# Kernel tuning notes

Hardware: AMD Instinct MI355X
Metric: run time of the kernel (lower is better)

The kernel has to match this reference:

```python
import jax, jax.numpy as jnp
import numpy as np

B, T, F, K = 32, 1500, 512, 31
QBITS = 8
EPS = 1e-5


def fake_quant(x, bits=QBITS):
    """Symmetric per-tensor fake quantization (scale from dynamic max-abs),
    with straight-through estimator so gradients pass through unchanged."""
    qmax = 2.0 ** (bits - 1) - 1.0  # 127 for 8 bits
    scale = jnp.maximum(jnp.max(jnp.abs(x)) / qmax, 1e-8)
    q = jnp.clip(jnp.round(x / scale), -qmax - 1.0, qmax) * scale
    return x + jax.lax.stop_gradient(q - x)


def setup_inputs() -> dict:
    key = jax.random.key(0)
    ks = jax.random.split(key, 5)
    x = jax.random.normal(ks[0], (B, T, F), dtype=jnp.float32)
    W1 = jax.random.normal(ks[1], (2 * F, F), dtype=jnp.float32) * (1.0 / np.sqrt(F))
    b1 = jnp.zeros((2 * F,), jnp.float32)
    dw_w = jax.random.normal(ks[2], (F, 1, K), dtype=jnp.float32) * (1.0 / np.sqrt(K))
    dw_b = jnp.zeros((F,), jnp.float32)
    W2 = jax.random.normal(ks[3], (F, F), dtype=jnp.float32) * (1.0 / np.sqrt(F))
    b2 = jnp.zeros((F,), jnp.float32)
    return {
        "x": x,
        "ln_gamma": jnp.ones((F,), jnp.float32),
        "ln_beta": jnp.zeros((F,), jnp.float32),
        "W1": W1, "b1": b1,
        "dw_w": dw_w, "dw_b": dw_b,
        "bn_gamma": jnp.ones((F,), jnp.float32),
        "bn_beta": jnp.zeros((F,), jnp.float32),
        "W2": W2, "b2": b2,
    }


def _forward(x, ln_gamma, ln_beta, W1, b1, dw_w, dw_b, bn_gamma, bn_beta, W2, b2):
    # LayerNorm over last dim F
    mu = jnp.mean(x, axis=-1, keepdims=True)
    var = jnp.mean(jnp.square(x - mu), axis=-1, keepdims=True)
    t = (x - mu) * jax.lax.rsqrt(var + EPS) * ln_gamma + ln_beta

    # pconv1 in-quant -> quantized pointwise conv1 (Linear F -> 2F) -> out-quant
    t = fake_quant(t)
    t = jnp.einsum("btf,gf->btg", t, fake_quant(W1)) + b1
    t = fake_quant(t)

    # GLU over last dim: [B,T,2F] -> [B,T,F]
    a, g = jnp.split(t, 2, axis=-1)
    t = a * jax.nn.sigmoid(g)

    # depthwise conv on [B,F,T]
    t = jnp.transpose(t, (0, 2, 1))  # [B,F,T]
    t = fake_quant(t)
    t = jax.lax.conv_general_dilated(
        t, fake_quant(dw_w),
        window_strides=(1,),
        padding=[((K - 1) // 2, (K - 1) // 2)],
        feature_group_count=F,
        dimension_numbers=("NCH", "OIH", "NCH"),
    ) + dw_b[None, :, None]
    t = fake_quant(t)

    # BatchNorm1d over channel dim (stats over batch and time), training-style batch stats
    bmu = jnp.mean(t, axis=(0, 2), keepdims=True)
    bvar = jnp.mean(jnp.square(t - bmu), axis=(0, 2), keepdims=True)
    t = (t - bmu) * jax.lax.rsqrt(bvar + EPS) * bn_gamma[None, :, None] + bn_beta[None, :, None]

    t = jnp.transpose(t, (0, 2, 1))  # [B,T,F]
    t = jax.nn.silu(t)

    # pconv2 in-quant -> quantized pointwise conv2 (Linear F -> F) -> out-quant
    t = fake_quant(t)
    t = jnp.einsum("btf,gf->btg", t, fake_quant(W2)) + b2
    t = fake_quant(t)
    return t  # dropout is identity (p=0 / eval)


def reference(x, ln_gamma, ln_beta, W1, b1, dw_w, dw_b, bn_gamma, bn_beta, W2, b2):
    return _forward(x, ln_gamma, ln_beta, W1, b1, dw_w, dw_b, bn_gamma, bn_beta, W2, b2)
```

## Files before the change

### kernel.cpp

```cpp
#include <hip/hip_runtime.h>
#include <stdint.h>

typedef __bf16 bf16;
typedef float    fx4    __attribute__((ext_vector_type(4)));
typedef int      ix2    __attribute__((ext_vector_type(2)));
typedef int      ix4    __attribute__((ext_vector_type(4)));

#define NB 32
#define NT 1500
#define NF 512
#define NM (NB*NT)
#define KW 31
#define EPSF 1e-5f

__device__ __forceinline__ float dscale(const float* a) {
  return fmaxf(a[0] * (1.0f/127.0f), 1e-8f);
}
__device__ __forceinline__ float fq_int(float x, float inv_s) {
  return fminf(fmaxf(rintf(x*inv_s), -128.0f), 127.0f);
}
__device__ __forceinline__ void block_amax(float v, float* dst) {
  __shared__ float red[8];
  #pragma unroll
  for (int o = 32; o > 0; o >>= 1) v = fmaxf(v, __shfl_xor(v, o));
  if ((threadIdx.x & 63) == 0) red[threadIdx.x >> 6] = v;
  __syncthreads();
  if (threadIdx.x == 0) {
    int nw = blockDim.x >> 6;
    float m = red[0];
    for (int i = 1; i < nw; i++) m = fmaxf(m, red[i]);
    atomicMax((unsigned int*)dst, __float_as_uint(m));
  }
}

__device__ __forceinline__ float amax_loop(const float* p, long n4, int bid, int gsz) {
  float am = 0.f;
  long i = (long)bid * blockDim.x + threadIdx.x;
  long stride = (long)gsz * blockDim.x;
  for (; i < n4; i += stride) {
    fx4 v = ((const fx4*)p)[i];
    #pragma unroll
    for (int j = 0; j < 4; j++) am = fmaxf(am, fabsf(v[j]));
  }
  return am;
}
__global__ void absmax_w(const float* __restrict__ W1, const float* __restrict__ W2,
                         const float* __restrict__ dwp, float* a) {
  int bx = blockIdx.x;
  float am; float* dst;
  if (bx < 256)      { am = amax_loop(W1,  131072, bx,       256); dst = a + 1; }
  else if (bx < 384) { am = amax_loop(W2,  65536,  bx - 256, 128); dst = a + 2; }
  else               { am = amax_loop(dwp, 3968,   bx - 384, 8);   dst = a + 3; }
  block_amax(am, dst);
}

__global__ void quant_pack_i8(const float* __restrict__ src, char* __restrict__ dst,
                              int R, const float* amax) {
  float inv_s = 1.0f / dscale(amax);
  int total = R * 32;
  for (int t = blockIdx.x*blockDim.x + threadIdx.x; t < total; t += gridDim.x*blockDim.x) {
    int r = t >> 5, q16 = t & 31;
    const float* s = src + (size_t)r*512 + q16*16;
    ix4 o;
    #pragma unroll
    for (int g = 0; g < 4; g++) {
      fx4 v = *(const fx4*)(s + g*4);
      int wrd = 0;
      #pragma unroll
      for (int j = 0; j < 4; j++) wrd |= ((int)fq_int(v[j], inv_s) & 0xff) << (8*j);
      o[g] = wrd;
    }
    int r16 = r >> 4, m16 = r & 15, kb = q16 >> 2, quad = q16 & 3;
    size_t chunk = ((size_t)r16*8 + kb)*64 + quad*16 + m16;
    ((ix4*)dst)[chunk] = o;
  }
}

__global__ void quant_deq_f32(float* __restrict__ p, long n4, const float* amax) {
  float s = dscale(amax);
  float inv_s = 1.0f / s;
  long i = (long)blockIdx.x * blockDim.x + threadIdx.x;
  long stride = (long)gridDim.x * blockDim.x;
  for (; i < n4; i += stride) {
    fx4 v = ((fx4*)p)[i];
    fx4 o;
    #pragma unroll
    for (int j = 0; j < 4; j++) o[j] = fq_int(v[j], inv_s) * s;
    ((fx4*)p)[i] = o;
  }
}

__global__ void ln_amax_k(const float* __restrict__ x, const float* __restrict__ g,
                          const float* __restrict__ be, float* amax) {
  int lane = threadIdx.x & 63;
  int wavesTotal = (gridDim.x * blockDim.x) >> 6;
  int wave = ((blockIdx.x * blockDim.x) + threadIdx.x) >> 6;
  fx4 g0 = ((const fx4*)g)[2*lane],  g1 = ((const fx4*)g)[2*lane+1];
  fx4 b0 = ((const fx4*)be)[2*lane], b1v = ((const fx4*)be)[2*lane+1];
  float gf[8], bff[8];
  #pragma unroll
  for (int j = 0; j < 4; j++) { gf[j] = g0[j]; gf[4+j] = g1[j]; bff[j] = b0[j]; bff[4+j] = b1v[j]; }
  float am = 0.f;
  for (int row = wave; row < NM; row += wavesTotal) {
    const fx4* xr = (const fx4*)(x + (long)row*NF);
    fx4 x0 = xr[2*lane], x1 = xr[2*lane+1];
    float xf[8]; float s = 0.f;
    #pragma unroll
    for (int j = 0; j < 4; j++) { xf[j] = x0[j]; xf[4+j] = x1[j]; }
    #pragma unroll
    for (int j = 0; j < 8; j++) s += xf[j];
    #pragma unroll
    for (int o = 32; o > 0; o >>= 1) s += __shfl_xor(s, o);
    float mu = s * (1.0f/NF);
    float vs = 0.f;
    #pragma unroll
    for (int j = 0; j < 8; j++) { float d = xf[j]-mu; vs += d*d; }
    #pragma unroll
    for (int o = 32; o > 0; o >>= 1) vs += __shfl_xor(vs, o);
    float inv = rsqrtf(vs*(1.0f/NF) + EPSF);
    #pragma unroll
    for (int j = 0; j < 8; j++) {
      float v = (xf[j]-mu)*inv*gf[j] + bff[j];
      am = fmaxf(am, fabsf(v));
    }
  }
  block_amax(am, amax);
}

__global__ void ln_pack_k(const float* __restrict__ x, const float* __restrict__ g,
                          const float* __restrict__ be, char* __restrict__ dst,
                          const float* amax) {
  int lane = threadIdx.x & 63;
  int wavesTotal = (gridDim.x * blockDim.x) >> 6;
  int wave = ((blockIdx.x * blockDim.x) + threadIdx.x) >> 6;
  float inv_s = 1.0f / dscale(amax);
  fx4 g0 = ((const fx4*)g)[2*lane],  g1 = ((const fx4*)g)[2*lane+1];
  fx4 b0 = ((const fx4*)be)[2*lane], b1v = ((const fx4*)be)[2*lane+1];
  float gf[8], bff[8];
  #pragma unroll
  for (int j = 0; j < 4; j++) { gf[j] = g0[j]; gf[4+j] = g1[j]; bff[j] = b0[j]; bff[4+j] = b1v[j]; }
  for (int row = wave; row < NM; row += wavesTotal) {
    const fx4* xr = (const fx4*)(x + (long)row*NF);
    fx4 x0 = xr[2*lane], x1 = xr[2*lane+1];
    float xf[8]; float s = 0.f;
    #pragma unroll
    for (int j = 0; j < 4; j++) { xf[j] = x0[j]; xf[4+j] = x1[j]; }
    #pragma unroll
    for (int j = 0; j < 8; j++) s += xf[j];
    #pragma unroll
    for (int o = 32; o > 0; o >>= 1) s += __shfl_xor(s, o);
    float mu = s * (1.0f/NF);
    float vs = 0.f;
    #pragma unroll
    for (int j = 0; j < 8; j++) { float d = xf[j]-mu; vs += d*d; }
    #pragma unroll
    for (int o = 32; o > 0; o >>= 1) vs += __shfl_xor(vs, o);
    float inv = rsqrtf(vs*(1.0f/NF) + EPSF);
    int lo = 0, hi = 0;
    #pragma unroll
    for (int j = 0; j < 4; j++) {
      float v = (xf[j]-mu)*inv*gf[j] + bff[j];
      lo |= ((int)fq_int(v, inv_s) & 0xff) << (8*j);
    }
    #pragma unroll
    for (int j = 0; j < 4; j++) {
      float v = (xf[4+j]-mu)*inv*gf[4+j] + bff[4+j];
      hi |= ((int)fq_int(v, inv_s) & 0xff) << (8*j);
    }
    size_t chunk = ((size_t)(row>>4)*8 + (lane>>3))*64 + ((lane>>1)&3)*16 + (row&15);
    *(ix2*)(dst + chunk*16 + (lane&1)*8) = ix2{lo, hi};
  }
}

template<int NBN, int MODE>
__global__ __launch_bounds__(256) void gemm_k(
    const char* __restrict__ A, const char* __restrict__ Bt,
    const float* __restrict__ bias, float* __restrict__ C,
    const float* amaxA, const float* amaxB, float* amaxC) {
  const int N = NBN * 128;
  int id = blockIdx.x;
  int bn = (id >> 3) % NBN;
  int bm = 8 * (id / (8 * NBN)) + (id & 7);
  if (bm >= 375) return;
  int lane = threadIdx.x & 63;
  int w = threadIdx.x >> 6;
  int wm = w >> 1, wn = w & 1;
  int quad = lane >> 4;
  int m16 = lane & 15;

  __shared__ __align__(16) float ebuf[2][32][132];

  ix4 acc[4][4];
  #pragma unroll
  for (int i = 0; i < 4; i++)
    #pragma unroll
    for (int j = 0; j < 4; j++) acc[i][j] = ix4{0,0,0,0};

  const char* pA[4];
  const char* pB[4];
  #pragma unroll
  for (int i = 0; i < 4; i++)
    pA[i] = A + (size_t)(bm*8 + wm*4 + i)*8192 + lane*16;
  #pragma unroll
  for (int j = 0; j < 4; j++)
    pB[j] = Bt + (size_t)(bn*8 + wn*4 + j)*8192 + lane*16;

  #pragma unroll
  for (int kb = 0; kb < 8; kb++) {
    ix4 aF[4], bF[4];
    #pragma unroll
    for (int i = 0; i < 4; i++) aF[i] = *(const ix4*)(pA[i] + kb*1024);
    #pragma unroll
    for (int j = 0; j < 4; j++) bF[j] = *(const ix4*)(pB[j] + kb*1024);
    #pragma unroll
    for (int i = 0; i < 4; i++)
      #pragma unroll
      for (int j = 0; j < 4; j++) {
        if (MODE == 0)
          acc[i][j] = __builtin_amdgcn_mfma_i32_16x16x64_i8(aF[i], bF[j], acc[i][j], 0, 0, 0);
        else
          acc[i][j] = __builtin_amdgcn_mfma_i32_16x16x64_i8(bF[j], aF[i], acc[i][j], 0, 0, 0);
      }
  }

  float ab = dscale(amaxA) * dscale(amaxB);
  float am = 0.f;
  const int h     = (MODE == 0) ? wn : wm;
  const int other = (MODE == 0) ? wm : wn;

  #pragma unroll
  for (int rnd = 0; rnd < 2; rnd++) {
    __syncthreads();
    if (MODE == 0) {
      #pragma unroll
      for (int jj = 0; jj < 2; jj++) {
        int j = rnd*2 + jj;
        int col = bn*128 + wn*64 + j*16 + m16;
        float bv = bias[col];
        #pragma unroll
        for (int i = 0; i < 4; i++) {
          fx4 o;
          #pragma unroll
          for (int rr = 0; rr < 4; rr++) {
            float v = (float)acc[i][j][rr]*ab + bv;
            am = fmaxf(am, fabsf(v)); o[rr] = v;
          }
          *(fx4*)&ebuf[h][jj*16 + m16][wm*64 + i*16 + quad*4] = o;
        }
      }
    } else {
      #pragma unroll
      for (int ii = 0; ii < 2; ii++) {
        int i = rnd*2 + ii;
        #pragma unroll
        for (int j = 0; j < 4; j++) {
          int n0 = bn*128 + wn*64 + j*16 + quad*4;
          fx4 bv = *(const fx4*)(bias + n0);
          fx4 o;
          #pragma unroll
          for (int rr = 0; rr < 4; rr++) {
            float v = (float)acc[i][j][rr]*ab + bv[rr];
            am = fmaxf(am, fabsf(v)); o[rr] = v;
          }
          *(fx4*)&ebuf[h][ii*16 + m16][wn*64 + j*16 + quad*4] = o;
        }
      }
    }
    __syncthreads();
    #pragma unroll
    for (int it = 0; it < 8; it++) {
      int lrow = other*16 + it*2 + (lane >> 5);
      int cf = (lane & 31) * 4;
      fx4 o = *(const fx4*)&ebuf[h][lrow][cf];
      int orow = ((MODE == 0) ? bn*128 : bm*128) + h*64 + rnd*32 + lrow;
      size_t base = (MODE == 0) ? ((size_t)orow*NM + (size_t)bm*128 + cf)
                                : ((size_t)orow*N  + (size_t)bn*128 + cf);
      *(fx4*)(C + base) = o;
    }
  }
  block_amax(am, amaxC);
}

__global__ void glu_k(const float* __restrict__ uT, float* __restrict__ v,
                      const float* amaxU, float* amaxV) {
  float s = dscale(amaxU);
  float inv_s = 1.0f / s;
  float am = 0.f;
  const int tid = threadIdx.x;
  const int npairs = (NB*NF)/2;
  for (int pr = blockIdx.x; pr < npairs; pr += gridDim.x) {
    int row0 = pr*2;
    for (int i = tid; i < 750; i += 256) {
      int r2 = (i >= 375) ? 1 : 0;
      int c = i - 375*r2;
      int row = row0 + r2;
      int b = row >> 9, f = row & (NF-1);
      long bt = (long)b*NT + c*4;
      fx4 a = *(const fx4*)(uT + (long)f*NM + bt);
      fx4 g = *(const fx4*)(uT + (long)(f+NF)*NM + bt);
      fx4 o;
      #pragma unroll
      for (int j = 0; j < 4; j++) {
        float av = fq_int(a[j], inv_s) * s;
        float gv = fq_int(g[j], inv_s) * s;
        float val = av * (1.0f/(1.0f + expf(-gv)));
        am = fmaxf(am, fabsf(val));
        o[j] = val;
      }
      *(fx4*)(v + (long)row*NT + c*4) = o;
    }
  }
  block_amax(am, amaxV);
}

__global__ void dwconv_k(const float* __restrict__ v, const float* __restrict__ w,
                         const float* __restrict__ wb, float* __restrict__ y,
                         const float* amaxV, const float* amaxW, float* amaxY) {
  __shared__ float z[2][1568];
  __shared__ float wl[2][32];
  float sv = dscale(amaxV); float inv_sv = 1.0f/sv;
  float sw = dscale(amaxW); float inv_sw = 1.0f/sw;
  float am = 0.f;
  const int tid = threadIdx.x;
  const int rr = tid >> 7;
  const int cl = tid & 127;
  const int wr2 = tid >> 5, wkk = tid & 31;

  if (tid < 128) {
    int r2 = tid >> 6, jj = tid & 63;
    if (jj < 16) z[r2][jj] = 0.f;
    else         z[r2][1500 + jj] = 0.f;
  }

  fx4 st[3];
  float wreg = 0.f;

  {
    long vb = (long)(blockIdx.x*2) * NT;
    #pragma unroll
    for (int k = 0; k < 3; k++) {
      int i = tid + k*256;
      if (i < 750) st[k] = *(const fx4*)(v + vb + i*4);
    }
    if (tid < 64 && wkk < KW)
      wreg = w[((blockIdx.x*2 + wr2) & (NF-1))*KW + wkk];
    #pragma unroll
    for (int k = 0; k < 3; k++) {
      int i = tid + k*256;
      if (i < 750) {
        int r2 = (i >= 375) ? 1 : 0;
        int ii = i - 375*r2;
        fx4 o;
        #pragma unroll
        for (int j = 0; j < 4; j++) o[j] = fq_int(st[k][j], inv_sv) * sv;
        *(fx4*)&z[r2][16 + 4*ii] = o;
      }
    }
    if (tid < 64 && wkk < KW) wl[wr2][wkk] = fq_int(wreg, inv_sw) * sw;
  }
  __syncthreads();

  #pragma unroll
  for (int idx = 0; idx < 4; idx++) {
    int p = blockIdx.x + idx*2048;
    if (idx < 3) {
      long vb = (long)((p + 2048)*2) * NT;
      #pragma unroll
      for (int k = 0; k < 3; k++) {
        int i = tid + k*256;
        if (i < 750) st[k] = *(const fx4*)(v + vb + i*4);
      }
      if (tid < 64 && wkk < KW)
        wreg = w[(((p + 2048)*2 + wr2) & (NF-1))*KW + wkk];
    }
    float wr[KW];
    #pragma unroll
    for (int k = 0; k < KW; k++) wr[k] = wl[rr][k];
    float bias = wb[(p*2 + rr) & (NF-1)];
    long base = (long)(p*2 + rr) * NT;
    #pragma unroll
    for (int pass = 0; pass < 3; pass++) {
      int c = cl + pass*128;
      if (c < 375) {
        int t0 = c*4;
        fx4 win[9];
        #pragma unroll
        for (int i = 0; i < 9; i++) win[i] = *(const fx4*)&z[rr][t0 + 4*i];
        float acc0 = bias, acc1 = bias, acc2 = bias, acc3 = bias;
        #pragma unroll
        for (int k = 0; k < KW; k++) {
          float wk = wr[k];
          acc0 += win[(k+1)>>2][(k+1)&3] * wk;
          acc1 += win[(k+2)>>2][(k+2)&3] * wk;
          acc2 += win[(k+3)>>2][(k+3)&3] * wk;
          acc3 += win[(k+4)>>2][(k+4)&3] * wk;
        }
        fx4 o = {acc0, acc1, acc2, acc3};
        #pragma unroll
        for (int j = 0; j < 4; j++) am = fmaxf(am, fabsf(o[j]));
        *(fx4*)&y[base + t0] = o;
      }
    }
    __syncthreads();
    if (idx < 3) {
      #pragma unroll
      for (int k = 0; k < 3; k++) {
        int i = tid + k*256;
        if (i < 750) {
          int r2 = (i >= 375) ? 1 : 0;
          int ii = i - 375*r2;
          fx4 o;
          #pragma unroll
          for (int j = 0; j < 4; j++) o[j] = fq_int(st[k][j], inv_sv) * sv;
          *(fx4*)&z[r2][16 + 4*ii] = o;
        }
      }
      if (tid < 64 && wkk < KW) wl[wr2][wkk] = fq_int(wreg, inv_sw) * sw;
      __syncthreads();
    }
  }
  block_amax(am, amaxY);
}

__global__ void bnstats_part_k(const float* __restrict__ y, const float* amaxY,
                               int* s1a, int* s2a, unsigned* qmxa, unsigned* qmna) {
  float sy = dscale(amaxY); float inv_sy = 1.0f/sy;
  int f = blockIdx.x & 511;
  int part = blockIdx.x >> 9;
  int s1 = 0, s2 = 0, qmn = 127, qmx = -128;
  for (int b = part*8; b < part*8 + 8; b++) {
    const fx4* base = (const fx4*)(y + ((long)b*NF + f)*NT);
    for (int i = threadIdx.x; i < NT/4; i += blockDim.x) {
      fx4 v = base[i];
      #pragma unroll
      for (int j = 0; j < 4; j++) {
        int q = (int)fq_int(v[j], inv_sy);
        s1 += q; s2 += q*q;
        qmn = min(qmn, q); qmx = max(qmx, q);
      }
    }
  }
  #pragma unroll
  for (int o = 32; o > 0; o >>= 1) {
    s1 += __shfl_xor(s1, o); s2 += __shfl_xor(s2, o);
    qmn = min(qmn, __shfl_xor(qmn, o)); qmx = max(qmx, __shfl_xor(qmx, o));
  }
  __shared__ int rs1[4], rs2[4], rmn[4], rmx[4];
  if ((threadIdx.x & 63) == 0) {
    int wv = threadIdx.x >> 6;
    rs1[wv] = s1; rs2[wv] = s2; rmn[wv] = qmn; rmx[wv] = qmx;
  }
  __syncthreads();
  if (threadIdx.x == 0) {
    int S1 = rs1[0]+rs1[1]+rs1[2]+rs1[3];
    int S2 = rs2[0]+rs2[1]+rs2[2]+rs2[3];
    int mn = min(min(rmn[0],rmn[1]), min(rmn[2],rmn[3]));
    int mx = max(max(rmx[0],rmx[1]), max(rmx[2],rmx[3]));
    atomicAdd(s1a + f, S1);
    atomicAdd(s2a + f, S2);
    atomicMax(qmxa + f, (unsigned)(mx + 128));
    atomicMax(qmna + f, (unsigned)(127 - mn));
  }
}

__global__ void bnfin_k(const int* __restrict__ s1a, const int* __restrict__ s2a,
                        const unsigned* __restrict__ qmxa, const unsigned* __restrict__ qmna,
                        const float* amaxY, const float* __restrict__ bg,
                        const float* __restrict__ bb,
                        float* bn_mean, float* bn_rinv, float* amaxP) {
  int f = blockIdx.x;
  float sy = dscale(amaxY);
  __shared__ float sh_mean, sh_rinv; __shared__ int sh_qmn, sh_qmx;
  if (threadIdx.x == 0) {
    long long S1 = s1a[f];
    long long S2 = s2a[f];
    double s = (double)sy;
    double mean = (double)S1 * s / (double)NM;
    double var  = (double)S2 * s * s / (double)NM - mean*mean;
    float fm = (float)mean;
    float fr = rsqrtf((float)var + EPSF);
    bn_mean[f] = fm; bn_rinv[f] = fr;
    sh_mean = fm; sh_rinv = fr;
    sh_qmx = (int)qmxa[f] - 128;
    sh_qmn = 127 - (int)qmna[f];
  }
  __syncthreads();
  float pm = 0.f;
  int q = sh_qmn + (int)threadIdx.x;
  if (q <= sh_qmx) {
    float zq = (float)q * sy;
    float val = (zq - sh_mean)*sh_rinv*bg[f] + bb[f];
    val = val / (1.0f + expf(-val));
    pm = fabsf(val);
  }
  block_amax(pm, amaxP);
}

__global__ void bnsilu_pack_k(const float* __restrict__ y, const float* __restrict__ bg,
                              const float* __restrict__ bb, const float* amaxY,
                              const float* bn_mean, const float* bn_rinv,
                              char* __restrict__ pq, const float* amaxP) {
  __shared__ float lds[32][33];
  float sy = dscale(amaxY); float inv_sy = 1.0f/sy;
  float inv_sp = 1.0f / dscale(amaxP);
  int tx = threadIdx.x & 31, ty = threadIdx.x >> 5;
  const int TTILES = (NT + 31)/32;
  const int ntile = NB * (NF/32) * TTILES;
  for (int tile = blockIdx.x; tile < ntile; tile += gridDim.x) {
    int b = tile / ((NF/32)*TTILES);
    int rem = tile % ((NF/32)*TTILES);
    int fT = rem / TTILES, tT = rem % TTILES;
    int f0 = fT*32, t0 = tT*32;
    __syncthreads();
    #pragma unroll
    for (int sI = 0; sI < 4; sI++) {
      int f = f0 + ty + sI*8;
      int t = t0 + tx;
      if (t < NT) {
        float zq = fq_int(y[((long)b*NF + f)*NT + t], inv_sy) * sy;
        float val = (zq - bn_mean[f])*bn_rinv[f]*bg[f] + bb[f];
        val = val / (1.0f + expf(-val));
        lds[tx][ty + sI*8] = val;
      }
    }
    __syncthreads();
    if (threadIdx.x < 128) {
      int r = threadIdx.x >> 2;
      int c = threadIdx.x & 3;
      int t = t0 + r;
      if (t < NT) {
        int lo = 0, hi = 0;
        #pragma unroll
        for (int j = 0; j < 4; j++)
          lo |= ((int)fq_int(lds[r][c*8 + j],     inv_sp) & 0xff) << (8*j);
        #pragma unroll
        for (int j = 0; j < 4; j++)
          hi |= ((int)fq_int(lds[r][c*8 + 4 + j], inv_sp) & 0xff) << (8*j);
        long bt = (long)b*NT + t;
        int q8 = (f0 >> 3) + c;
        size_t chunk = ((size_t)(bt>>4)*8 + (q8>>3))*64 + ((q8>>1)&3)*16 + (bt&15);
        *(ix2*)(pq + chunk*16 + (q8&1)*8) = ix2{lo, hi};
      }
    }
  }
}

extern "C" void kernel_launch(void* const* d_in, const int* in_sizes, int n_in,
                              void* d_out, int out_size, void* d_ws, size_t ws_size,
                              hipStream_t stream) {
  const float* x  = (const float*)d_in[0];
  const float* lg = (const float*)d_in[1];
  const float* lb = (const float*)d_in[2];
  const float* W1 = (const float*)d_in[3];
  const float* b1 = (const float*)d_in[4];
  const float* dw = (const float*)d_in[5];
  const float* db = (const float*)d_in[6];
  const float* bg = (const float*)d_in[7];
  const float* bb = (const float*)d_in[8];
  const float* W2 = (const float*)d_in[9];
  const float* b2 = (const float*)d_in[10];
  float* out = (float*)d_out;

  char* ws = (char*)d_ws;
  float* amax    = (float*)ws;
  float* bn_mean = (float*)(ws + 1024);
  float* bn_rinv = (float*)(ws + 4096);
  int*      s1a  = (int*)(ws + 8192);
  int*      s2a  = (int*)(ws + 10240);
  unsigned* qmxa = (unsigned*)(ws + 12288);
  unsigned* qmna = (unsigned*)(ws + 14336);
  char* H = ws + 16384;
  float* uT    = (float*)H;
  char*  t_q   = H + 196608000;
  float* y     = (float*)H;
  char*  p_q   = H + 221184000;
  char*  W1q   = H + 245760000;
  char*  W2q   = H + 246284288;
  float* v = (float*)d_out;
  float* r = (float*)d_out;

  hipMemsetAsync(ws, 0, 16384, stream);

  absmax_w<<<392, 256, 0, stream>>>(W1, W2, dw, amax);
  quant_pack_i8<<<128, 256, 0, stream>>>(W1, W1q, 1024, amax+1);
  quant_pack_i8<<<64,  256, 0, stream>>>(W2, W2q, 512,  amax+2);

  ln_amax_k<<<1536, 256, 0, stream>>>(x, lg, lb, amax+0);
  ln_pack_k<<<3072, 256, 0, stream>>>(x, lg, lb, t_q, amax+0);
  gemm_k<8,0><<<3008, 256, 0, stream>>>(t_q, W1q, b1, uT, amax+0, amax+1, amax+4);
  glu_k<<<4096, 256, 0, stream>>>(uT, v, amax+4, amax+5);
  dwconv_k<<<2048, 256, 0, stream>>>(v, dw, db, y, amax+5, amax+3, amax+6);
  bnstats_part_k<<<2048, 256, 0, stream>>>(y, amax+6, s1a, s2a, qmxa, qmna);
  bnfin_k<<<512, 256, 0, stream>>>(s1a, s2a, qmxa, qmna, amax+6, bg, bb, bn_mean, bn_rinv, amax+7);
  bnsilu_pack_k<<<4096, 256, 0, stream>>>(y, bg, bb, amax+6, bn_mean, bn_rinv, p_q, amax+7);
  gemm_k<4,1><<<1504, 256, 0, stream>>>(p_q, W2q, b2, r, amax+7, amax+2, amax+8);
  quant_deq_f32<<<2048, 256, 0, stream>>>(out, 24576000/4, amax+8);
}
```

Before: 548.7 us.

## Restructure depthwise conv to one row per wave and merge weight-pack launches

The depthwise conv kernel now gives each wavefront its own row in shared memory: four rows per block, two rows per wave in total, with no block-level barriers. Before, the whole block cooperated on two rows across four iterations, with __syncthreads between them. The next row is still prefetched into registers while the current one is computed. The two weight quantize-pack launches are merged into a single kernel, saving a launch. Fewer rows per block and more blocks resident per CU may change latency hiding, and the prefetch registers (st[6]) raise register pressure.

```diff
diff --git a/kernel.cpp b/kernel.cpp
--- a/kernel.cpp
+++ b/kernel.cpp
@@ -54,11 +54,10 @@
   block_amax(am, dst);
 }
 
-__global__ void quant_pack_i8(const float* __restrict__ src, char* __restrict__ dst,
-                              int R, const float* amax) {
-  float inv_s = 1.0f / dscale(amax);
+__device__ __forceinline__ void qp_body(const float* __restrict__ src, char* __restrict__ dst,
+                                        int R, float inv_s, int bid, int gsz) {
   int total = R * 32;
-  for (int t = blockIdx.x*blockDim.x + threadIdx.x; t < total; t += gridDim.x*blockDim.x) {
+  for (int t = bid*256 + threadIdx.x; t < total; t += gsz*256) {
     int r = t >> 5, q16 = t & 31;
     const float* s = src + (size_t)r*512 + q16*16;
     ix4 o;
@@ -74,6 +73,12 @@
     size_t chunk = ((size_t)r16*8 + kb)*64 + quad*16 + m16;
     ((ix4*)dst)[chunk] = o;
   }
+}
+__global__ void quant_pack_w(const float* __restrict__ W1, const float* __restrict__ W2,
+                             char* __restrict__ W1q, char* __restrict__ W2q,
+                             const float* amax) {
+  if (blockIdx.x < 128) qp_body(W1, W1q, 1024, 1.0f/dscale(amax+1), blockIdx.x, 128);
+  else                  qp_body(W2, W2q, 512,  1.0f/dscale(amax+2), blockIdx.x-128, 64);
 }
 
 __global__ void quant_deq_f32(float* __restrict__ p, long n4, const float* amax) {
@@ -316,107 +321,117 @@
 __global__ void dwconv_k(const float* __restrict__ v, const float* __restrict__ w,
                          const float* __restrict__ wb, float* __restrict__ y,
                          const float* amaxV, const float* amaxW, float* amaxY) {
-  __shared__ float z[2][1568];
-  __shared__ float wl[2][32];
+  __shared__ float z[4][1536];
+  __shared__ float wl[4][32];
   float sv = dscale(amaxV); float inv_sv = 1.0f/sv;
   float sw = dscale(amaxW); float inv_sw = 1.0f/sw;
   float am = 0.f;
-  const int tid = threadIdx.x;
-  const int rr = tid >> 7;
-  const int cl = tid & 127;
-  const int wr2 = tid >> 5, wkk = tid & 31;
-
-  if (tid < 128) {
-    int r2 = tid >> 6, jj = tid & 63;
-    if (jj < 16) z[r2][jj] = 0.f;
-    else         z[r2][1500 + jj] = 0.f;
-  }
-
-  fx4 st[3];
+  const int wave = threadIdx.x >> 6, lane = threadIdx.x & 63;
+  float* zz = z[wave];
+
+  if (lane < 16) zz[lane] = 0.f;
+  else if (lane < 32) zz[1500 + lane] = 0.f;
+
+  const int rowA = blockIdx.x*4 + wave;
+  const int rowB = rowA + 8192;
+
+  fx4 st[6];
   float wreg = 0.f;
 
   {
-    long vb = (long)(blockIdx.x*2) * NT;
-    #pragma unroll
-    for (int k = 0; k < 3; k++) {
-      int i = tid + k*256;
-      if (i < 750) st[k] = *(const fx4*)(v + vb + i*4);
-    }
-    if (tid < 64 && wkk < KW)
-      wreg = w[((blockIdx.x*2 + wr2) & (NF-1))*KW + wkk];
-    #pragma unroll
-    for (int k = 0; k < 3; k++) {
-      int i = tid + k*256;
-      if (i < 750) {
-        int r2 = (i >= 375) ? 1 : 0;
-        int ii = i - 375*r2;
+    long vb = (long)rowA * NT;
+    #pragma unroll
+    for (int k = 0; k < 6; k++) { int i = lane + k*64; if (i < 375) st[k] = *(const fx4*)(v + vb + i*4); }
+    if (lane < KW) wreg = w[(rowA & (NF-1))*KW + lane];
+    #pragma unroll
+    for (int k = 0; k < 6; k++) {
+      int i = lane + k*64;
+      if (i < 375) {
         fx4 o;
         #pragma unroll
         for (int j = 0; j < 4; j++) o[j] = fq_int(st[k][j], inv_sv) * sv;
-        *(fx4*)&z[r2][16 + 4*ii] = o;
-      }
-    }
-    if (tid < 64 && wkk < KW) wl[wr2][wkk] = fq_int(wreg, inv_sw) * sw;
-  }
-  __syncthreads();
-
-  #pragma unroll
-  for (int idx = 0; idx < 4; idx++) {
-    int p = blockIdx.x + idx*2048;
-    if (idx < 3) {
-      long vb = (long)((p + 2048)*2) * NT;
-      #pragma unroll
-      for (int k = 0; k < 3; k++) {
-        int i = tid + k*256;
-        if (i < 750) st[k] = *(const fx4*)(v + vb + i*4);
-      }
-      if (tid < 64 && wkk < KW)
-        wreg = w[(((p + 2048)*2 + wr2) & (NF-1))*KW + wkk];
-    }
+        *(fx4*)&zz[16 + 4*i] = o;
+      }
+    }
+    if (lane < KW) wl[wave][lane] = fq_int(wreg, inv_sw) * sw;
+  }
+  {
+    long vb = (long)rowB * NT;
+    #pragma unroll
+    for (int k = 0; k < 6; k++) { int i = lane + k*64; if (i < 375) st[k] = *(const fx4*)(v + vb + i*4); }
+    if (lane < KW) wreg = w[(rowB & (NF-1))*KW + lane];
+  }
+  {
     float wr[KW];
     #pragma unroll
-    for (int k = 0; k < KW; k++) wr[k] = wl[rr][k];
-    float bias = wb[(p*2 + rr) & (NF-1)];
-    long base = (long)(p*2 + rr) * NT;
-    #pragma unroll
-    for (int pass = 0; pass < 3; pass++) {
-      int c = cl + pass*128;
+    for (int k = 0; k < KW; k++) wr[k] = wl[wave][k];
+    float bias = wb[rowA & (NF-1)];
+    long base = (long)rowA * NT;
+    #pragma unroll
+    for (int p = 0; p < 6; p++) {
+      int c = lane + p*64;
       if (c < 375) {
         int t0 = c*4;
         fx4 win[9];
         #pragma unroll
-        for (int i = 0; i < 9; i++) win[i] = *(const fx4*)&z[rr][t0 + 4*i];
-        float acc0 = bias, acc1 = bias, acc2 = bias, acc3 = bias;
+        for (int i = 0; i < 9; i++) win[i] = *(const fx4*)&zz[t0 + 4*i];
+        float a0 = bias, a1 = bias, a2 = bias, a3 = bias;
         #pragma unroll
         for (int k = 0; k < KW; k++) {
           float wk = wr[k];
-          acc0 += win[(k+1)>>2][(k+1)&3] * wk;
-          acc1 += win[(k+2)>>2][(k+2)&3] * wk;
-          acc2 += win[(k+3)>>2][(k+3)&3] * wk;
-          acc3 += win[(k+4)>>2][(k+4)&3] * wk;
+          a0 += win[(k+1)>>2][(k+1)&3] * wk;
+          a1 += win[(k+2)>>2][(k+2)&3] * wk;
+          a2 += win[(k+3)>>2][(k+3)&3] * wk;
+          a3 += win[(k+4)>>2][(k+4)&3] * wk;
         }
-        fx4 o = {acc0, acc1, acc2, acc3};
+        fx4 o = {a0, a1, a2, a3};
         #pragma unroll
         for (int j = 0; j < 4; j++) am = fmaxf(am, fabsf(o[j]));
         *(fx4*)&y[base + t0] = o;
       }
     }
-    __syncthreads();
-    if (idx < 3) {
-      #pragma unroll
-      for (int k = 0; k < 3; k++) {
-        int i = tid + k*256;
-        if (i < 750) {
-          int r2 = (i >= 375) ? 1 : 0;
-          int ii = i - 375*r2;
-          fx4 o;
-          #pragma unroll
-          for (int j = 0; j < 4; j++) o[j] = fq_int(st[k][j], inv_sv) * sv;
-          *(fx4*)&z[r2][16 + 4*ii] = o;
+  }
+  {
+    #pragma unroll
+    for (int k = 0; k < 6; k++) {
+      int i = lane + k*64;
+      if (i < 375) {
+        fx4 o;
+        #pragma unroll
+        for (int j = 0; j < 4; j++) o[j] = fq_int(st[k][j], inv_sv) * sv;
+        *(fx4*)&zz[16 + 4*i] = o;
+      }
+    }
+    if (lane < KW) wl[wave][lane] = fq_int(wreg, inv_sw) * sw;
+  }
+  {
+    float wr[KW];
+    #pragma unroll
+    for (int k = 0; k < KW; k++) wr[k] = wl[wave][k];
+    float bias = wb[rowB & (NF-1)];
+    long base = (long)rowB * NT;
+    #pragma unroll
+    for (int p = 0; p < 6; p++) {
+      int c = lane + p*64;
+      if (c < 375) {
+        int t0 = c*4;
+        fx4 win[9];
+        #pragma unroll
+        for (int i = 0; i < 9; i++) win[i] = *(const fx4*)&zz[t0 + 4*i];
+        float a0 = bias, a1 = bias, a2 = bias, a3 = bias;
+        #pragma unroll
+        for (int k = 0; k < KW; k++) {
+          float wk = wr[k];
+          a0 += win[(k+1)>>2][(k+1)&3] * wk;
+          a1 += win[(k+2)>>2][(k+2)&3] * wk;
+          a2 += win[(k+3)>>2][(k+3)&3] * wk;
+          a3 += win[(k+4)>>2][(k+4)&3] * wk;
         }
-      }
-      if (tid < 64 && wkk < KW) wl[wr2][wkk] = fq_int(wreg, inv_sw) * sw;
-      __syncthreads();
+        fx4 o = {a0, a1, a2, a3};
+        #pragma unroll
+        for (int j = 0; j < 4; j++) am = fmaxf(am, fabsf(o[j]));
+        *(fx4*)&y[base + t0] = o;
+      }
     }
   }
   block_amax(am, amaxY);
@@ -582,8 +597,7 @@
   hipMemsetAsync(ws, 0, 16384, stream);
 
   absmax_w<<<392, 256, 0, stream>>>(W1, W2, dw, amax);
-  quant_pack_i8<<<128, 256, 0, stream>>>(W1, W1q, 1024, amax+1);
-  quant_pack_i8<<<64,  256, 0, stream>>>(W2, W2q, 512,  amax+2);
+  quant_pack_w<<<192, 256, 0, stream>>>(W1, W2, W1q, W2q, amax);
 
   ln_amax_k<<<1536, 256, 0, stream>>>(x, lg, lb, amax+0);
   ln_pack_k<<<3072, 256, 0, stream>>>(x, lg, lb, t_q, amax+0);
```

After: 563.4 us. 1.03x slower.
